# Kernel optimization log

Hardware: AMD Instinct MI355X
Metric: run time of the kernel (lower is better)

## Reference

```python
import jax, jax.numpy as jnp
import numpy as np


def _renorm(e):
    # torch Embedding max_norm=1: clip each looked-up vector to L2 norm <= 1
    n = jnp.linalg.norm(e, axis=-1, keepdims=True)
    return e * jnp.minimum(1.0, 1.0 / jnp.maximum(n, 1e-12))


def _lstm_last(x, lens, Wih, Whh, bih, bhh):
    # x: [N, T, D]; returns hidden state at step lens-1 per sequence
    N, T, D = x.shape
    tmask = jnp.arange(T)[None, :] < lens[:, None]  # [N, T]
    b = bih + bhh

    def step(carry, inp):
        h, c = carry
        xt, m = inp  # [N, D], [N]
        gates = xt @ Wih.T + h @ Whh.T + b
        i, f, g, o = jnp.split(gates, 4, axis=-1)
        c_new = jax.nn.sigmoid(f) * c + jax.nn.sigmoid(i) * jnp.tanh(g)
        h_new = jax.nn.sigmoid(o) * jnp.tanh(c_new)
        m = m[:, None]
        return (jnp.where(m, h_new, h), jnp.where(m, c_new, c)), None

    h0 = jnp.zeros((N, D), x.dtype)
    (hn, _), _ = jax.lax.scan(step, (h0, h0), (jnp.transpose(x, (1, 0, 2)), tmask.T))
    return hn


def _gat(feat, src, dst, idx_map, W, b, n_dst):
    # edge dot-product score + edge softmax over dst + weighted scatter-sum
    fd = feat[idx_map]                                   # [n_dst, D]
    score = jnp.sum(feat[src] * fd[dst], axis=-1)        # [E]
    m = jax.ops.segment_max(score, dst, num_segments=n_dst)
    w = jnp.exp(score - m[dst])
    z = jax.ops.segment_sum(w, dst, num_segments=n_dst)
    w = w / jnp.maximum(z[dst], 1e-12)
    agg = jax.ops.segment_sum(w[:, None] * feat[src], dst, num_segments=n_dst)
    rst = jax.nn.relu(agg @ W.T + b)
    return fd + rst  # residual=True


def setup_inputs() -> dict:
    key = jax.random.key(0)
    ks = jax.random.split(key, 24)
    D = 128
    N0, N1, N2 = 25600, 2560, 512
    E0, E1 = 25600, 5120
    T = 20
    NU, NI = 100000, 50000
    s = 0.05
    inp = {
        "user_emb": jax.random.normal(ks[0], (NU, D), jnp.float32),
        "item_emb": jax.random.normal(ks[1], (NI + 1, D), jnp.float32),
        "Wih": jax.random.normal(ks[2], (4 * D, D), jnp.float32) * s,
        "Whh": jax.random.normal(ks[3], (4 * D, D), jnp.float32) * s,
        "bih": jax.random.normal(ks[4], (4 * D,), jnp.float32) * s,
        "bhh": jax.random.normal(ks[5], (4 * D,), jnp.float32) * s,
        "W1": jax.random.normal(ks[6], (D, 2 * D), jnp.float32) * s,
        "gW0": jax.random.normal(ks[7], (D, D), jnp.float32) * s,
        "gb0": jax.random.normal(ks[8], (D,), jnp.float32) * s,
        "gW1": jax.random.normal(ks[9], (D, D), jnp.float32) * s,
        "gb1": jax.random.normal(ks[10], (D,), jnp.float32) * s,
        "W2": jax.random.normal(ks[11], (D, 2 * D), jnp.float32) * s,
        "uids": jax.random.randint(ks[12], (N0,), 0, NU, jnp.int32),
        "padded_seqs": jax.random.randint(ks[13], (N0, T), 0, NI + 1, jnp.int32),
        "lens": jax.random.randint(ks[14], (N0,), 1, T + 1, jnp.int32),
        "cur_sidx": jax.random.randint(ks[15], (N2,), 0, N0, jnp.int32),
        "src0": jax.random.randint(ks[16], (E0,), 0, N0, jnp.int32),
        "dst0": jax.random.randint(ks[17], (E0,), 0, N1, jnp.int32),
        "idx0": jax.random.randint(ks[18], (N1,), 0, N0, jnp.int32),
        "src1": jax.random.randint(ks[19], (E1,), 0, N1, jnp.int32),
        "dst1": jax.random.randint(ks[20], (E1,), 0, N2, jnp.int32),
        "idx1": jax.random.randint(ks[21], (N2,), 0, N1, jnp.int32),
    }
    return inp


def reference(user_emb, item_emb, Wih, Whh, bih, bhh, W1, gW0, gb0, gW1, gb1, W2,
              uids, padded_seqs, lens, cur_sidx, src0, dst0, idx0, src1, dst1, idx1):
    item_emb = item_emb.at[0].set(0.0)  # padding_idx=0
    emb_seqs = _renorm(item_emb[padded_seqs])             # [N0, T, D]
    hn = _lstm_last(emb_seqs, lens, Wih, Whh, bih, bhh)   # [N0, D] short-term
    long_term = _renorm(user_emb[uids])                   # [N0, D]
    cur = hn[cur_sidx]                                    # [B, D]
    feat = jax.nn.relu(jnp.concatenate([long_term, hn], axis=1) @ W1.T)
    feat = feat.at[cur_sidx].set(cur)
    feat = _gat(feat, src0, dst0, idx0, gW0, gb0, idx0.shape[0])
    feat = _gat(feat, src1, dst1, idx1, gW1, gb1, idx1.shape[0])
    sr = jnp.concatenate([cur, feat], axis=1) @ W2.T      # [B, D]
    logits = sr @ _renorm(item_emb[1:]).T                 # [B, num_items]
    return logits
```

## Files before the change

### kernel.cpp

```cpp
#include <hip/hip_runtime.h>
#include <hip/hip_bf16.h>

typedef __bf16 bf16x8 __attribute__((ext_vector_type(8)));
typedef float  f32x4  __attribute__((ext_vector_type(4)));

__device__ __forceinline__ float fastsig(float x){
  return __builtin_amdgcn_rcpf(1.f + __builtin_amdgcn_exp2f(-1.4426950408889634f * x));
}
__device__ __forceinline__ float fasttanh(float x){
  return 1.f - 2.f * __builtin_amdgcn_rcpf(__builtin_amdgcn_exp2f(2.8853900817779268f * x) + 1.f);
}

__device__ __forceinline__ unsigned encf(float f){
  unsigned u = __float_as_uint(f);
  return (u & 0x80000000u) ? ~u : (u | 0x80000000u);
}
__device__ __forceinline__ float decf(unsigned u){
  return __uint_as_float((u & 0x80000000u) ? (u ^ 0x80000000u) : ~u);
}

__device__ __forceinline__ int swzG(int row, int byteoff){ return ((row<<7) + byteoff) ^ ((row & 7) << 4); }

__global__ void init_kernel(unsigned* agg0, unsigned* agg1, unsigned* z0, unsigned* z1,
                            unsigned* m0, unsigned* m1, unsigned* hist){
  int g = blockIdx.x*256 + threadIdx.x;
  if      (g < 327680)                          agg0[g] = 0u;
  else if ((g -= 327680) < 65536)               agg1[g] = 0u;
  else if ((g -= 65536)  < 2560)                z0[g]   = 0u;
  else if ((g -= 2560)   < 512)                 z1[g]   = 0u;
  else if ((g -= 512)    < 2560)                m0[g]   = 0x00800000u;
  else if ((g -= 2560)   < 512)                 m1[g]   = 0x00800000u;
  else if ((g -= 512)    < 20)                  hist[g] = 0u;
}

__global__ void len_hist_kernel(const int* __restrict__ lens, int* __restrict__ hist, int n){
  __shared__ int lh[20];
  int t = threadIdx.x;
  if (t < 20) lh[t] = 0;
  __syncthreads();
  int i = blockIdx.x*256 + t;
  if (i < n) atomicAdd(&lh[lens[i]-1], 1);
  __syncthreads();
  if (t < 20 && lh[t] > 0) atomicAdd(&hist[t], lh[t]);
}
__global__ void len_prefix_kernel(const int* __restrict__ hist, int* __restrict__ offs){
  if (threadIdx.x == 0){
    int acc = 0;
    for (int i = 19; i >= 0; --i){ offs[i] = acc; acc += hist[i]; }
  }
}
__global__ void len_scatter_kernel(const int* __restrict__ lens, int* __restrict__ offs,
                                   int* __restrict__ perm, int n){
  __shared__ int cnt[20];
  __shared__ int base[20];
  int t = threadIdx.x;
  if (t < 20) cnt[t] = 0;
  __syncthreads();
  int i = blockIdx.x*256 + t;
  int bin = 0, rank = 0;
  if (i < n){
    bin = lens[i] - 1;
    rank = atomicAdd(&cnt[bin], 1);
  }
  __syncthreads();
  if (t < 20 && cnt[t] > 0) base[t] = atomicAdd(&offs[t], cnt[t]);
  __syncthreads();
  if (i < n) perm[base[bin] + rank] = i;
}

__global__ void prep_kernel(const float* __restrict__ Wih, const float* __restrict__ Whh,
                            const float* __restrict__ bih, const float* __restrict__ bhh,
                            const float* __restrict__ W1,
                            __bf16* __restrict__ Wcat, float* __restrict__ bias,
                            __bf16* __restrict__ W1b){
  int g = blockIdx.x*256 + threadIdx.x;
  if (g < 131072){
    int j = g >> 8, k = g & 255;
    float v = (k < 128) ? Wih[j*128 + k] : Whh[j*128 + (k-128)];
    Wcat[g] = (__bf16)v;
  } else if (g < 131584){
    int j = g - 131072;
    bias[j] = bih[j] + bhh[j];
  } else if (g < 164352){
    int q = g - 131584;
    W1b[q] = (__bf16)W1[q];
  }
}

__global__ void gather2_kernel(const float* __restrict__ item_emb, const float* __restrict__ user_emb,
                               const int* __restrict__ uids,
                               __bf16* __restrict__ itn, __bf16* __restrict__ A1){
  int r = blockIdx.x*4 + (threadIdx.x >> 6);
  if (r >= 75600) return;
  int lane = threadIdx.x & 63;
  const float* src;
  __bf16* dst;
  if (r < 50000){
    src = item_emb + (size_t)(r + 1)*128;
    dst = itn + (size_t)r*128;
  } else {
    int i = r - 50000;
    src = user_emb + (size_t)uids[i]*128;
    dst = A1 + (size_t)i*256;
  }
  float2 v = *(const float2*)(src + lane*2);
  float ss = v.x*v.x + v.y*v.y;
  #pragma unroll
  for (int m = 1; m < 64; m <<= 1) ss += __shfl_xor(ss, m);
  float scale = (ss > 1.f) ? (1.f/sqrtf(ss)) : 1.f;
  dst[lane*2]     = (__bf16)(v.x*scale);
  dst[lane*2 + 1] = (__bf16)(v.y*scale);
}

#define ROWB 528
__global__ __launch_bounds__(512, 1)
void lstm_kernel(const __bf16* __restrict__ itn, const int* __restrict__ seqs,
                 const __bf16* __restrict__ Wcat, const float* __restrict__ bias,
                 const int* __restrict__ lens, const int* __restrict__ perm,
                 __bf16* __restrict__ A1){
  __shared__ char Ab[64*ROWB];
  __shared__ float bsh[512];
  __shared__ int   llen[64];

  const int tid  = threadIdx.x;
  const int lane = tid & 63;
  const int wv   = tid >> 6;
  const int l15  = lane & 15;
  const int lq   = lane >> 4;
  const int n0   = blockIdx.x * 64;

  bsh[tid] = bias[tid];
  if (tid < 64) llen[tid] = lens[perm[n0 + tid]];

  const __bf16* wp[4];
  #pragma unroll
  for (int gi = 0; gi < 4; ++gi)
    wp[gi] = Wcat + (size_t)((gi*128 + wv*16 + l15)*256 + lq*8);

  const int xrow = tid >> 3;
  const int xsub = tid & 7;
  const int xwr  = xrow*ROWB + xsub*32;
  const int hwr  = xrow*ROWB + 256 + xsub*32;
  const int sidx = perm[n0 + xrow];

  __syncthreads();

  const int mxl = llen[0];
  int lens_p = 0;
  #pragma unroll
  for (int s = 0; s < 4; ++s)
    lens_p |= llen[s*16 + l15] << (8*s);

  float c[4][4];
  #pragma unroll
  for (int s = 0; s < 4; ++s)
    #pragma unroll
    for (int r = 0; r < 4; ++r) c[s][r] = 0.f;

  int rbs[4], hws[4];
  #pragma unroll
  for (int s = 0; s < 4; ++s){
    rbs[s] = (s*16 + l15)*ROWB + lq*16;
    hws[s] = (s*16 + l15)*ROWB + 256 + (wv*16 + lq*4)*2;
  }

  {
    const int4 z = {0,0,0,0};
    *(int4*)(Ab + hwr)      = z;
    *(int4*)(Ab + hwr + 16) = z;
    int idx0 = seqs[(size_t)sidx*20 + 0];
    int4 a = z, b = z;
    if (idx0 > 0){
      const __bf16* sp = itn + (size_t)(idx0-1)*128 + xsub*16;
      a = *(const int4*)(sp);
      b = *(const int4*)(sp + 8);
    }
    *(int4*)(Ab + xwr)      = a;
    *(int4*)(Ab + xwr + 16) = b;
  }
  int idx_next = seqs[(size_t)sidx*20 + 1];
  __syncthreads();

  for (int t = 0; t < mxl; ++t){
    int4 xq0 = {0,0,0,0}, xq1 = {0,0,0,0};
    const bool stage_next = (t + 1 < mxl);
    if (stage_next && idx_next > 0){
      const __bf16* sp = itn + (size_t)(idx_next-1)*128 + xsub*16;
      xq0 = *(const int4*)(sp);
      xq1 = *(const int4*)(sp + 8);
    }
    if (t + 2 < 20) idx_next = seqs[(size_t)sidx*20 + t + 2];

    f32x4 acc[4][4];
    #pragma unroll
    for (int gi = 0; gi < 4; ++gi){
      f32x4 bv = *(const f32x4*)(bsh + gi*128 + wv*16 + lq*4);
      #pragma unroll
      for (int s = 0; s < 4; ++s) acc[s][gi] = bv;
    }

    int4 s0[4], s1[4];
    #pragma unroll
    for (int gi = 0; gi < 4; ++gi) s0[gi] = *(const int4*)(wp[gi]);
    #pragma unroll
    for (int kk = 0; kk < 8; ++kk){
      if (kk < 7){
        if (kk & 1){
          #pragma unroll
          for (int gi = 0; gi < 4; ++gi) s0[gi] = *(const int4*)(wp[gi] + (kk+1)*32);
        } else {
          #pragma unroll
          for (int gi = 0; gi < 4; ++gi) s1[gi] = *(const int4*)(wp[gi] + (kk+1)*32);
        }
      }
      bf16x8 bfr[4];
      #pragma unroll
      for (int s = 0; s < 4; ++s)
        bfr[s] = __builtin_bit_cast(bf16x8, *(const int4*)(Ab + rbs[s] + kk*64));
      #pragma unroll
      for (int gi = 0; gi < 4; ++gi){
        bf16x8 wf = __builtin_bit_cast(bf16x8, (kk & 1) ? s1[gi] : s0[gi]);
        #pragma unroll
        for (int s = 0; s < 4; ++s)
          acc[s][gi] = __builtin_amdgcn_mfma_f32_16x16x32_bf16(wf, bfr[s], acc[s][gi], 0,0,0);
      }
    }

    float hv[4][4];
    #pragma unroll
    for (int s = 0; s < 4; ++s){
      const bool up = t < ((lens_p >> (8*s)) & 255);
      #pragma unroll
      for (int r = 0; r < 4; ++r){
        float cn = fastsig(acc[s][1][r])*c[s][r] + fastsig(acc[s][0][r])*fasttanh(acc[s][2][r]);
        hv[s][r] = fastsig(acc[s][3][r])*fasttanh(cn);
        if (up) c[s][r] = cn;
      }
    }

    __syncthreads();

    #pragma unroll
    for (int s = 0; s < 4; ++s){
      if (t < ((lens_p >> (8*s)) & 255)){
        union { __bf16 h[4]; int2 q; } u;
        #pragma unroll
        for (int r = 0; r < 4; ++r) u.h[r] = (__bf16)hv[s][r];
        *(int2*)(Ab + hws[s]) = u.q;
      }
    }
    if (stage_next){
      *(int4*)(Ab + xwr)      = xq0;
      *(int4*)(Ab + xwr + 16) = xq1;
    }
    __syncthreads();
  }

  {
    int4 a = *(const int4*)(Ab + hwr);
    int4 b = *(const int4*)(Ab + hwr + 16);
    __bf16* op = A1 + (size_t)sidx*256 + 128 + xsub*16;
    *(int4*)(op)     = a;
    *(int4*)(op + 8) = b;
  }
}

template<int RELU>
__global__ __launch_bounds__(256, 2)
void gemm_bt_kernel(const __bf16* __restrict__ A, const __bf16* __restrict__ B,
                    float* __restrict__ C, int M, int N, int K){
  __shared__ char As[16384];
  __shared__ char Bs[16384];
  const int tid  = threadIdx.x;
  const int lane = tid & 63;
  const int wv   = tid >> 6;
  const int wmw  = wv >> 1, wnw = wv & 1;
  const int l15  = lane & 15, lq = lane >> 4;
  const int n0 = blockIdx.x * 128;
  const int m0 = blockIdx.y * 128;

  f32x4 acc[4][4];
  #pragma unroll
  for (int a = 0; a < 4; ++a)
    #pragma unroll
    for (int b = 0; b < 4; ++b){ f32x4 z; z[0]=0.f;z[1]=0.f;z[2]=0.f;z[3]=0.f; acc[a][b]=z; }

  const int nkb = K >> 6;
  for (int kb = 0; kb < nkb; ++kb){
    __syncthreads();
    #pragma unroll
    for (int i = 0; i < 4; ++i){
      int c = tid + i*256;
      int row = c >> 3, kc = c & 7;
      int4 va = *(const int4*)(A + (size_t)(m0+row)*K + kb*64 + kc*8);
      *(int4*)(As + swzG(row, kc*16)) = va;
      int4 vb = {0,0,0,0};
      if (n0 + row < N) vb = *(const int4*)(B + (size_t)(n0+row)*K + kb*64 + kc*8);
      *(int4*)(Bs + swzG(row, kc*16)) = vb;
    }
    __syncthreads();
    #pragma unroll
    for (int ks = 0; ks < 2; ++ks){
      bf16x8 af[4], bfr[4];
      #pragma unroll
      for (int mi = 0; mi < 4; ++mi)
        af[mi] = __builtin_bit_cast(bf16x8, *(const int4*)(As + swzG(wmw*64 + mi*16 + l15, ks*64 + lq*16)));
      #pragma unroll
      for (int ni = 0; ni < 4; ++ni)
        bfr[ni] = __builtin_bit_cast(bf16x8, *(const int4*)(Bs + swzG(wnw*64 + ni*16 + l15, ks*64 + lq*16)));
      #pragma unroll
      for (int mi = 0; mi < 4; ++mi)
        #pragma unroll
        for (int ni = 0; ni < 4; ++ni)
          acc[mi][ni] = __builtin_amdgcn_mfma_f32_16x16x32_bf16(af[mi], bfr[ni], acc[mi][ni], 0,0,0);
    }
  }
  #pragma unroll
  for (int mi = 0; mi < 4; ++mi){
    #pragma unroll
    for (int ni = 0; ni < 4; ++ni){
      int col = n0 + wnw*64 + ni*16 + l15;
      if (col < N){
        #pragma unroll
        for (int r = 0; r < 4; ++r){
          int row = m0 + wmw*64 + mi*16 + lq*4 + r;
          float v = acc[mi][ni][r];
          if (RELU) v = fmaxf(v, 0.f);
          C[(size_t)row*N + col] = v;
        }
      }
    }
  }
}

__global__ void set_cur_kernel(const __bf16* __restrict__ A1, const int* __restrict__ cur_sidx,
                               float* __restrict__ feat){
  int g = blockIdx.x*256 + threadIdx.x;
  int i = g >> 7, d = g & 127;
  int row = cur_sidx[i];
  feat[(size_t)row*128 + d] = (float)A1[(size_t)row*256 + 128 + d];
}

__global__ void gat_score_kernel(const float* __restrict__ feat, const int* __restrict__ src,
                                 const int* __restrict__ dst, const int* __restrict__ idxm,
                                 float* __restrict__ score, unsigned* __restrict__ mbuf, int E){
  int e = blockIdx.x*4 + (threadIdx.x >> 6);
  if (e >= E) return;
  int lane = threadIdx.x & 63;
  int de = dst[e];
  const float2 a = *(const float2*)(feat + (size_t)src[e]*128 + lane*2);
  const float2 b = *(const float2*)(feat + (size_t)idxm[de]*128 + lane*2);
  float s = a.x*b.x + a.y*b.y;
  #pragma unroll
  for (int m = 1; m < 64; m <<= 1) s += __shfl_xor(s, m);
  if (lane == 0){
    score[e] = s;
    atomicMax(mbuf + de, encf(s));
  }
}

__global__ void gat_agg_kernel(const float* __restrict__ feat, const int* __restrict__ src,
                               const int* __restrict__ dst, const float* __restrict__ score,
                               const unsigned* __restrict__ mbuf,
                               float* __restrict__ agg, float* __restrict__ z, int E){
  int g = blockIdx.x*256 + threadIdx.x;
  int e = g >> 7, d = g & 127;
  if (e >= E) return;
  int de = dst[e];
  float w = __expf(score[e] - decf(mbuf[de]));
  if (d == 0) atomicAdd(z + de, w);
  atomicAdd(agg + (size_t)de*128 + d, w * feat[(size_t)src[e]*128 + d]);
}

__global__ void gat_out_kernel(const float* __restrict__ featPrev, const int* __restrict__ idxm,
                               const float* __restrict__ agg, const float* __restrict__ z,
                               const float* __restrict__ gW, const float* __restrict__ gb,
                               float* __restrict__ out, int V){
  __shared__ float arow[128];
  int v = blockIdx.x;
  int d = threadIdx.x;
  float zi = 1.f / fmaxf(z[v], 1e-12f);
  arow[d] = agg[(size_t)v*128 + d] * zi;
  __syncthreads();
  float s = gb[d];
  #pragma unroll 4
  for (int k = 0; k < 128; ++k) s += arow[k] * gW[d*128 + k];
  out[(size_t)v*128 + d] = featPrev[(size_t)idxm[v]*128 + d] + fmaxf(s, 0.f);
}

__global__ void sr_kernel(const __bf16* __restrict__ A1, const float* __restrict__ feat2,
                          const int* __restrict__ cur_sidx, const float* __restrict__ W2,
                          __bf16* __restrict__ srb){
  __shared__ float cat[256];
  int i = blockIdx.x;
  int j = threadIdx.x;
  int row = cur_sidx[i];
  cat[j]       = (float)A1[(size_t)row*256 + 128 + j];
  cat[128 + j] = feat2[(size_t)i*128 + j];
  __syncthreads();
  float s = 0.f;
  #pragma unroll 4
  for (int k = 0; k < 256; ++k) s += cat[k] * W2[j*256 + k];
  srb[(size_t)i*128 + j] = (__bf16)s;
}

extern "C" void kernel_launch(void* const* d_in, const int* in_sizes, int n_in,
                              void* d_out, int out_size, void* d_ws, size_t ws_size,
                              hipStream_t stream){
  const float* user_emb = (const float*)d_in[0];
  const float* item_emb = (const float*)d_in[1];
  const float* Wih = (const float*)d_in[2];
  const float* Whh = (const float*)d_in[3];
  const float* bih = (const float*)d_in[4];
  const float* bhh = (const float*)d_in[5];
  const float* W1  = (const float*)d_in[6];
  const float* gW0 = (const float*)d_in[7];
  const float* gb0 = (const float*)d_in[8];
  const float* gW1 = (const float*)d_in[9];
  const float* gb1 = (const float*)d_in[10];
  const float* W2  = (const float*)d_in[11];
  const int* uids = (const int*)d_in[12];
  const int* seqs = (const int*)d_in[13];
  const int* lens = (const int*)d_in[14];
  const int* cur_sidx = (const int*)d_in[15];
  const int* src0 = (const int*)d_in[16];
  const int* dst0 = (const int*)d_in[17];
  const int* idx0 = (const int*)d_in[18];
  const int* src1 = (const int*)d_in[19];
  const int* dst1 = (const int*)d_in[20];
  const int* idx1 = (const int*)d_in[21];
  float* out = (float*)d_out;

  char* ws = (char*)d_ws;
  size_t off = 0;
  auto alloc = [&](size_t bytes)->char* {
    char* p = ws + off;
    off += (bytes + 255) & ~((size_t)255);
    return p;
  };
  __bf16*   A1    = (__bf16*)  alloc(25600u*256*2);
  __bf16*   Wcat  = (__bf16*)  alloc(512u*256*2);
  float*    bias  = (float*)   alloc(512u*4);
  __bf16*   W1b   = (__bf16*)  alloc(128u*256*2);
  float*    feat  = (float*)   alloc(25600u*128*4);
  float*    sc0   = (float*)   alloc(25600u*4);
  unsigned* m0    = (unsigned*)alloc(2560u*4);
  float*    z0    = (float*)   alloc(2560u*4);
  float*    agg0  = (float*)   alloc(2560u*128*4);
  float*    feat1 = (float*)   alloc(2560u*128*4);
  float*    sc1   = (float*)   alloc(5120u*4);
  unsigned* m1    = (unsigned*)alloc(512u*4);
  float*    z1    = (float*)   alloc(512u*4);
  float*    agg1  = (float*)   alloc(512u*128*4);
  float*    feat2 = (float*)   alloc(512u*128*4);
  __bf16*   srb   = (__bf16*)  alloc(512u*128*2);
  __bf16*   itn   = (__bf16*)  alloc(50000u*128*2);
  int*      hist  = (int*)     alloc(20u*4);
  int*      offs  = (int*)     alloc(20u*4);
  int*      perm  = (int*)     alloc(25600u*4);

  prep_kernel<<<642, 256, 0, stream>>>(Wih, Whh, bih, bhh, W1, Wcat, bias, W1b);
  init_kernel<<<1561, 256, 0, stream>>>((unsigned*)agg0, (unsigned*)agg1, (unsigned*)z0,
                                        (unsigned*)z1, m0, m1, (unsigned*)hist);

  len_hist_kernel   <<<100, 256, 0, stream>>>(lens, hist, 25600);
  len_prefix_kernel <<<1,    64, 0, stream>>>(hist, offs);
  len_scatter_kernel<<<100, 256, 0, stream>>>(lens, offs, perm, 25600);

  gather2_kernel<<<18900, 256, 0, stream>>>(item_emb, user_emb, uids, itn, A1);

  lstm_kernel<<<400, 512, 0, stream>>>(itn, seqs, Wcat, bias, lens, perm, A1);

  gemm_bt_kernel<1><<<dim3(1, 200), 256, 0, stream>>>(A1, W1b, feat, 25600, 128, 256);
  set_cur_kernel<<<256, 256, 0, stream>>>(A1, cur_sidx, feat);

  gat_score_kernel<<<6400, 256, 0, stream>>>(feat, src0, dst0, idx0, sc0, m0, 25600);
  gat_agg_kernel  <<<12800,256, 0, stream>>>(feat, src0, dst0, sc0, m0, agg0, z0, 25600);
  gat_out_kernel  <<<2560, 128, 0, stream>>>(feat, idx0, agg0, z0, gW0, gb0, feat1, 2560);

  gat_score_kernel<<<1280, 256, 0, stream>>>(feat1, src1, dst1, idx1, sc1, m1, 5120);
  gat_agg_kernel  <<<2560, 256, 0, stream>>>(feat1, src1, dst1, sc1, m1, agg1, z1, 5120);
  gat_out_kernel  <<<512,  128, 0, stream>>>(feat1, idx1, agg1, z1, gW1, gb1, feat2, 512);

  sr_kernel<<<512, 128, 0, stream>>>(A1, feat2, cur_sidx, W2, srb);

  gemm_bt_kernel<0><<<dim3(391, 4), 256, 0, stream>>>(srb, itn, out, 512, 50000, 128);
}
```

Measured before the change: 265.2 us.

## Double-buffer LSTM shared state with swizzled layout to drop a barrier per step

The LSTM kernel now keeps two swizzled LDS buffers for the x/h operand and alternates between them each timestep. That removes the mid-step __syncthreads, and rows that are already finished copy their old h forward. The padded 528-byte row stride is replaced by an XOR swizzle against bank conflicts. Bias is now added after the MFMAs from global memory instead of LDS, and the first weight fragment is prefetched across steps. Max length comes from a wave shuffle rather than LDS. The cost is twice the LDS footprint, extra copy traffic for inactive rows, and repeated bias loads every step.

```diff
diff --git a/kernel.cpp b/kernel.cpp
--- a/kernel.cpp
+++ b/kernel.cpp
@@ -19,6 +19,7 @@
   return __uint_as_float((u & 0x80000000u) ? (u ^ 0x80000000u) : ~u);
 }
 
+__device__ __forceinline__ int swzA(int row, int byteoff){ return ((row<<9) + byteoff) ^ ((row & 7) << 4); }
 __device__ __forceinline__ int swzG(int row, int byteoff){ return ((row<<7) + byteoff) ^ ((row & 7) << 4); }
 
 __global__ void init_kernel(unsigned* agg0, unsigned* agg1, unsigned* z0, unsigned* z1,
@@ -112,15 +113,12 @@
   dst[lane*2 + 1] = (__bf16)(v.y*scale);
 }
 
-#define ROWB 528
 __global__ __launch_bounds__(512, 1)
 void lstm_kernel(const __bf16* __restrict__ itn, const int* __restrict__ seqs,
                  const __bf16* __restrict__ Wcat, const float* __restrict__ bias,
                  const int* __restrict__ lens, const int* __restrict__ perm,
                  __bf16* __restrict__ A1){
-  __shared__ char Ab[64*ROWB];
-  __shared__ float bsh[512];
-  __shared__ int   llen[64];
+  __shared__ char Ab[2][32768];
 
   const int tid  = threadIdx.x;
   const int lane = tid & 63;
@@ -129,45 +127,50 @@
   const int lq   = lane >> 4;
   const int n0   = blockIdx.x * 64;
 
-  bsh[tid] = bias[tid];
-  if (tid < 64) llen[tid] = lens[perm[n0 + tid]];
-
   const __bf16* wp[4];
   #pragma unroll
   for (int gi = 0; gi < 4; ++gi)
     wp[gi] = Wcat + (size_t)((gi*128 + wv*16 + l15)*256 + lq*8);
 
+  int lens_p = 0;
+  #pragma unroll
+  for (int s = 0; s < 4; ++s)
+    lens_p |= lens[perm[n0 + s*16 + l15]] << (8*s);
+  int mxl;
+  {
+    int m = max(max(lens_p & 255, (lens_p >> 8) & 255),
+                max((lens_p >> 16) & 255, (lens_p >> 24) & 255));
+    #pragma unroll
+    for (int o = 1; o < 16; o <<= 1) m = max(m, __shfl_xor(m, o));
+    mxl = m;
+  }
+
+  float c[4][4];
+  #pragma unroll
+  for (int s = 0; s < 4; ++s)
+    #pragma unroll
+    for (int r = 0; r < 4; ++r) c[s][r] = 0.f;
+
+  const int b64 = (l15 & 4) << 4;
+
+  int rbs[4], hws[4];
+  #pragma unroll
+  for (int s = 0; s < 4; ++s){
+    rbs[s] = swzA(s*16 + l15, lq*16) - b64;
+    hws[s] = swzA(s*16 + l15, 256 + (wv*16 + lq*4)*2);
+  }
   const int xrow = tid >> 3;
   const int xsub = tid & 7;
-  const int xwr  = xrow*ROWB + xsub*32;
-  const int hwr  = xrow*ROWB + 256 + xsub*32;
+  const int xwr0 = swzA(xrow, xsub*32);
+  const int xwr1 = swzA(xrow, xsub*32 + 16);
+  const int hwr0 = swzA(xrow, 256 + xsub*32);
+  const int hwr1 = swzA(xrow, 256 + xsub*32 + 16);
   const int sidx = perm[n0 + xrow];
-
-  __syncthreads();
-
-  const int mxl = llen[0];
-  int lens_p = 0;
-  #pragma unroll
-  for (int s = 0; s < 4; ++s)
-    lens_p |= llen[s*16 + l15] << (8*s);
-
-  float c[4][4];
-  #pragma unroll
-  for (int s = 0; s < 4; ++s)
-    #pragma unroll
-    for (int r = 0; r < 4; ++r) c[s][r] = 0.f;
-
-  int rbs[4], hws[4];
-  #pragma unroll
-  for (int s = 0; s < 4; ++s){
-    rbs[s] = (s*16 + l15)*ROWB + lq*16;
-    hws[s] = (s*16 + l15)*ROWB + 256 + (wv*16 + lq*4)*2;
-  }
 
   {
     const int4 z = {0,0,0,0};
-    *(int4*)(Ab + hwr)      = z;
-    *(int4*)(Ab + hwr + 16) = z;
+    *(int4*)(Ab[0] + hwr0) = z;
+    *(int4*)(Ab[0] + hwr1) = z;
     int idx0 = seqs[(size_t)sidx*20 + 0];
     int4 a = z, b = z;
     if (idx0 > 0){
@@ -175,13 +178,21 @@
       a = *(const int4*)(sp);
       b = *(const int4*)(sp + 8);
     }
-    *(int4*)(Ab + xwr)      = a;
-    *(int4*)(Ab + xwr + 16) = b;
+    *(int4*)(Ab[0] + xwr0) = a;
+    *(int4*)(Ab[0] + xwr1) = b;
   }
   int idx_next = seqs[(size_t)sidx*20 + 1];
+
+  int4 s0[4], s1[4];
+  #pragma unroll
+  for (int gi = 0; gi < 4; ++gi) s0[gi] = *(const int4*)(wp[gi]);
+
   __syncthreads();
 
   for (int t = 0; t < mxl; ++t){
+    const char* Bc = Ab[t & 1];
+    char*       Bn = Ab[(t & 1) ^ 1];
+
     int4 xq0 = {0,0,0,0}, xq1 = {0,0,0,0};
     const bool stage_next = (t + 1 < mxl);
     if (stage_next && idx_next > 0){
@@ -193,15 +204,10 @@
 
     f32x4 acc[4][4];
     #pragma unroll
-    for (int gi = 0; gi < 4; ++gi){
-      f32x4 bv = *(const f32x4*)(bsh + gi*128 + wv*16 + lq*4);
-      #pragma unroll
-      for (int s = 0; s < 4; ++s) acc[s][gi] = bv;
-    }
-
-    int4 s0[4], s1[4];
-    #pragma unroll
-    for (int gi = 0; gi < 4; ++gi) s0[gi] = *(const int4*)(wp[gi]);
+    for (int s = 0; s < 4; ++s)
+      #pragma unroll
+      for (int gi = 0; gi < 4; ++gi){ f32x4 z; z[0]=0.f;z[1]=0.f;z[2]=0.f;z[3]=0.f; acc[s][gi]=z; }
+
     #pragma unroll
     for (int kk = 0; kk < 8; ++kk){
       if (kk < 7){
@@ -213,10 +219,11 @@
           for (int gi = 0; gi < 4; ++gi) s1[gi] = *(const int4*)(wp[gi] + (kk+1)*32);
         }
       }
+      const int koff = (kk*64) ^ b64;
       bf16x8 bfr[4];
       #pragma unroll
       for (int s = 0; s < 4; ++s)
-        bfr[s] = __builtin_bit_cast(bf16x8, *(const int4*)(Ab + rbs[s] + kk*64));
+        bfr[s] = __builtin_bit_cast(bf16x8, *(const int4*)(Bc + rbs[s] + koff));
       #pragma unroll
       for (int gi = 0; gi < 4; ++gi){
         bf16x8 wf = __builtin_bit_cast(bf16x8, (kk & 1) ? s1[gi] : s0[gi]);
@@ -226,39 +233,49 @@
       }
     }
 
-    float hv[4][4];
-    #pragma unroll
-    for (int s = 0; s < 4; ++s){
-      const bool up = t < ((lens_p >> (8*s)) & 255);
-      #pragma unroll
-      for (int r = 0; r < 4; ++r){
-        float cn = fastsig(acc[s][1][r])*c[s][r] + fastsig(acc[s][0][r])*fasttanh(acc[s][2][r]);
-        hv[s][r] = fastsig(acc[s][3][r])*fasttanh(cn);
-        if (up) c[s][r] = cn;
-      }
-    }
-
-    __syncthreads();
+    if (stage_next){
+      #pragma unroll
+      for (int gi = 0; gi < 4; ++gi) s0[gi] = *(const int4*)(wp[gi]);
+    }
+
+    float bb[4][4];
+    #pragma unroll
+    for (int gi = 0; gi < 4; ++gi)
+      #pragma unroll
+      for (int r = 0; r < 4; ++r)
+        bb[gi][r] = bias[gi*128 + wv*16 + lq*4 + r];
 
     #pragma unroll
     for (int s = 0; s < 4; ++s){
       if (t < ((lens_p >> (8*s)) & 255)){
         union { __bf16 h[4]; int2 q; } u;
         #pragma unroll
-        for (int r = 0; r < 4; ++r) u.h[r] = (__bf16)hv[s][r];
-        *(int2*)(Ab + hws[s]) = u.q;
+        for (int r = 0; r < 4; ++r){
+          float ig = acc[s][0][r] + bb[0][r];
+          float fg = acc[s][1][r] + bb[1][r];
+          float gg = acc[s][2][r] + bb[2][r];
+          float og = acc[s][3][r] + bb[3][r];
+          float cn = fastsig(fg)*c[s][r] + fastsig(ig)*fasttanh(gg);
+          u.h[r] = (__bf16)(fastsig(og)*fasttanh(cn));
+          c[s][r] = cn;
+        }
+        *(int2*)(Bn + hws[s]) = u.q;
+      } else {
+        *(int2*)(Bn + hws[s]) = *(const int2*)(Bc + hws[s]);
       }
     }
+
     if (stage_next){
-      *(int4*)(Ab + xwr)      = xq0;
-      *(int4*)(Ab + xwr + 16) = xq1;
+      *(int4*)(Bn + xwr0) = xq0;
+      *(int4*)(Bn + xwr1) = xq1;
     }
     __syncthreads();
   }
 
   {
-    int4 a = *(const int4*)(Ab + hwr);
-    int4 b = *(const int4*)(Ab + hwr + 16);
+    const char* fb = Ab[mxl & 1];
+    int4 a = *(const int4*)(fb + hwr0);
+    int4 b = *(const int4*)(fb + hwr1);
     __bf16* op = A1 + (size_t)sidx*256 + 128 + xsub*16;
     *(int4*)(op)     = a;
     *(int4*)(op + 8) = b;
```

Measured after the change: 319.8 us. +20.6%, slower.

## Replace atomic GAT scatter with CSR-by-destination segment reduction fused into output

Applied to the files above, without the earlier changes.

Builds a destination-sorted edge order (histogram, prefix scan, scatter) for both GAT layers, then computes the segment max, softmax normaliser and weighted aggregation per destination node inside the output kernel. This removes the float atomicAdd scatter into agg/z, the atomicMax pass and the large zero-initialisation of agg buffers. In exchange it adds six small sort kernels and serial per-node edge loops whose length depends on degree skew.

```diff
diff --git a/kernel.cpp b/kernel.cpp
--- a/kernel.cpp
+++ b/kernel.cpp
@@ -11,26 +11,13 @@
   return 1.f - 2.f * __builtin_amdgcn_rcpf(__builtin_amdgcn_exp2f(2.8853900817779268f * x) + 1.f);
 }
 
-__device__ __forceinline__ unsigned encf(float f){
-  unsigned u = __float_as_uint(f);
-  return (u & 0x80000000u) ? ~u : (u | 0x80000000u);
-}
-__device__ __forceinline__ float decf(unsigned u){
-  return __uint_as_float((u & 0x80000000u) ? (u ^ 0x80000000u) : ~u);
-}
-
 __device__ __forceinline__ int swzG(int row, int byteoff){ return ((row<<7) + byteoff) ^ ((row & 7) << 4); }
 
-__global__ void init_kernel(unsigned* agg0, unsigned* agg1, unsigned* z0, unsigned* z1,
-                            unsigned* m0, unsigned* m1, unsigned* hist){
+__global__ void init_kernel(int* dh0, int* dh1, int* lhist){
   int g = blockIdx.x*256 + threadIdx.x;
-  if      (g < 327680)                          agg0[g] = 0u;
-  else if ((g -= 327680) < 65536)               agg1[g] = 0u;
-  else if ((g -= 65536)  < 2560)                z0[g]   = 0u;
-  else if ((g -= 2560)   < 512)                 z1[g]   = 0u;
-  else if ((g -= 512)    < 2560)                m0[g]   = 0x00800000u;
-  else if ((g -= 2560)   < 512)                 m1[g]   = 0x00800000u;
-  else if ((g -= 512)    < 20)                  hist[g] = 0u;
+  if      (g < 2560)            dh0[g]   = 0;
+  else if ((g -= 2560) < 512)   dh1[g]   = 0;
+  else if ((g -= 512)  < 20)    lhist[g] = 0;
 }
 
 __global__ void len_hist_kernel(const int* __restrict__ lens, int* __restrict__ hist, int n){
@@ -66,6 +53,55 @@
   if (t < 20 && cnt[t] > 0) base[t] = atomicAdd(&offs[t], cnt[t]);
   __syncthreads();
   if (i < n) perm[base[bin] + rank] = i;
+}
+
+__global__ void dst_hist_kernel(const int* __restrict__ dst, int* __restrict__ hist,
+                                int E, int nbins){
+  __shared__ int lh[2560];
+  int t = threadIdx.x;
+  for (int b = t; b < nbins; b += 256) lh[b] = 0;
+  __syncthreads();
+  int i = blockIdx.x*256 + t;
+  if (i < E) atomicAdd(&lh[dst[i]], 1);
+  __syncthreads();
+  for (int b = t; b < nbins; b += 256){ int v = lh[b]; if (v) atomicAdd(&hist[b], v); }
+}
+__global__ void dst_prefix_kernel(const int* __restrict__ hist, int* __restrict__ starts,
+                                  int* __restrict__ cur, int nbins){
+  __shared__ int wsum[4];
+  int t = threadIdx.x;
+  int per = nbins >> 8;
+  int base = t*per;
+  int loc = 0;
+  for (int i = 0; i < per; ++i) loc += hist[base+i];
+  int lane = t & 63, wid = t >> 6;
+  int scan = loc;
+  #pragma unroll
+  for (int o = 1; o < 64; o <<= 1){ int v = __shfl_up(scan, o); if (lane >= o) scan += v; }
+  if (lane == 63) wsum[wid] = scan;
+  __syncthreads();
+  int woff = 0;
+  for (int w = 0; w < wid; ++w) woff += wsum[w];
+  int run = woff + scan - loc;
+  for (int i = 0; i < per; ++i){
+    starts[base+i] = run; cur[base+i] = run; run += hist[base+i];
+  }
+  if (t == 255) starts[nbins] = run;
+}
+__global__ void dst_scatter_kernel(const int* __restrict__ dst, int* __restrict__ cur,
+                                   int* __restrict__ eord, int E, int nbins){
+  __shared__ int cnt[2560];
+  __shared__ int base[2560];
+  int t = threadIdx.x;
+  for (int b = t; b < nbins; b += 256) cnt[b] = 0;
+  __syncthreads();
+  int i = blockIdx.x*256 + t;
+  int bin = 0, rank = 0;
+  if (i < E){ bin = dst[i]; rank = atomicAdd(&cnt[bin], 1); }
+  __syncthreads();
+  for (int b = t; b < nbins; b += 256){ int v = cnt[b]; if (v) base[b] = atomicAdd(&cur[b], v); }
+  __syncthreads();
+  if (i < E) eord[base[bin] + rank] = i;
 }
 
 __global__ void prep_kernel(const float* __restrict__ Wih, const float* __restrict__ Whh,
@@ -343,7 +379,7 @@
 
 __global__ void gat_score_kernel(const float* __restrict__ feat, const int* __restrict__ src,
                                  const int* __restrict__ dst, const int* __restrict__ idxm,
-                                 float* __restrict__ score, unsigned* __restrict__ mbuf, int E){
+                                 float* __restrict__ score, int E){
   int e = blockIdx.x*4 + (threadIdx.x >> 6);
   if (e >= E) return;
   int lane = threadIdx.x & 63;
@@ -353,39 +389,33 @@
   float s = a.x*b.x + a.y*b.y;
   #pragma unroll
   for (int m = 1; m < 64; m <<= 1) s += __shfl_xor(s, m);
-  if (lane == 0){
-    score[e] = s;
-    atomicMax(mbuf + de, encf(s));
-  }
-}
-
-__global__ void gat_agg_kernel(const float* __restrict__ feat, const int* __restrict__ src,
-                               const int* __restrict__ dst, const float* __restrict__ score,
-                               const unsigned* __restrict__ mbuf,
-                               float* __restrict__ agg, float* __restrict__ z, int E){
-  int g = blockIdx.x*256 + threadIdx.x;
-  int e = g >> 7, d = g & 127;
-  if (e >= E) return;
-  int de = dst[e];
-  float w = __expf(score[e] - decf(mbuf[de]));
-  if (d == 0) atomicAdd(z + de, w);
-  atomicAdd(agg + (size_t)de*128 + d, w * feat[(size_t)src[e]*128 + d]);
-}
-
-__global__ void gat_out_kernel(const float* __restrict__ featPrev, const int* __restrict__ idxm,
-                               const float* __restrict__ agg, const float* __restrict__ z,
-                               const float* __restrict__ gW, const float* __restrict__ gb,
-                               float* __restrict__ out, int V){
+  if (lane == 0) score[e] = s;
+}
+
+__global__ void gat_fused_kernel(const float* __restrict__ feat, const int* __restrict__ src,
+                                 const int* __restrict__ idxm, const float* __restrict__ score,
+                                 const int* __restrict__ eord, const int* __restrict__ starts,
+                                 const float* __restrict__ gW, const float* __restrict__ gb,
+                                 float* __restrict__ out, int V){
   __shared__ float arow[128];
   int v = blockIdx.x;
   int d = threadIdx.x;
-  float zi = 1.f / fmaxf(z[v], 1e-12f);
-  arow[d] = agg[(size_t)v*128 + d] * zi;
+  int e0 = starts[v], e1 = starts[v+1];
+  float m = -3.4e38f;
+  for (int i = e0; i < e1; ++i) m = fmaxf(m, score[eord[i]]);
+  float z = 0.f, acc = 0.f;
+  for (int i = e0; i < e1; ++i){
+    int e = eord[i];
+    float w = __expf(score[e] - m);
+    z += w;
+    acc += w * feat[(size_t)src[e]*128 + d];
+  }
+  arow[d] = acc * (1.f / fmaxf(z, 1e-12f));
   __syncthreads();
   float s = gb[d];
   #pragma unroll 4
   for (int k = 0; k < 128; ++k) s += arow[k] * gW[d*128 + k];
-  out[(size_t)v*128 + d] = featPrev[(size_t)idxm[v]*128 + d] + fmaxf(s, 0.f);
+  out[(size_t)v*128 + d] = feat[(size_t)idxm[v]*128 + d] + fmaxf(s, 0.f);
 }
 
 __global__ void sr_kernel(const __bf16* __restrict__ A1, const float* __restrict__ feat2,
@@ -444,29 +474,37 @@
   __bf16*   W1b   = (__bf16*)  alloc(128u*256*2);
   float*    feat  = (float*)   alloc(25600u*128*4);
   float*    sc0   = (float*)   alloc(25600u*4);
-  unsigned* m0    = (unsigned*)alloc(2560u*4);
-  float*    z0    = (float*)   alloc(2560u*4);
-  float*    agg0  = (float*)   alloc(2560u*128*4);
   float*    feat1 = (float*)   alloc(2560u*128*4);
   float*    sc1   = (float*)   alloc(5120u*4);
-  unsigned* m1    = (unsigned*)alloc(512u*4);
-  float*    z1    = (float*)   alloc(512u*4);
-  float*    agg1  = (float*)   alloc(512u*128*4);
   float*    feat2 = (float*)   alloc(512u*128*4);
   __bf16*   srb   = (__bf16*)  alloc(512u*128*2);
   __bf16*   itn   = (__bf16*)  alloc(50000u*128*2);
   int*      hist  = (int*)     alloc(20u*4);
   int*      offs  = (int*)     alloc(20u*4);
   int*      perm  = (int*)     alloc(25600u*4);
+  int*      dh0   = (int*)     alloc(2560u*4);
+  int*      st0   = (int*)     alloc(2561u*4);
+  int*      cur0  = (int*)     alloc(2560u*4);
+  int*      eord0 = (int*)     alloc(25600u*4);
+  int*      dh1   = (int*)     alloc(512u*4);
+  int*      st1   = (int*)     alloc(513u*4);
+  int*      cur1  = (int*)     alloc(512u*4);
+  int*      eord1 = (int*)     alloc(5120u*4);
 
   prep_kernel<<<642, 256, 0, stream>>>(Wih, Whh, bih, bhh, W1, Wcat, bias, W1b);
-  init_kernel<<<1561, 256, 0, stream>>>((unsigned*)agg0, (unsigned*)agg1, (unsigned*)z0,
-                                        (unsigned*)z1, m0, m1, (unsigned*)hist);
+  init_kernel<<<13, 256, 0, stream>>>(dh0, dh1, hist);
 
   len_hist_kernel   <<<100, 256, 0, stream>>>(lens, hist, 25600);
   len_prefix_kernel <<<1,    64, 0, stream>>>(hist, offs);
   len_scatter_kernel<<<100, 256, 0, stream>>>(lens, offs, perm, 25600);
 
+  dst_hist_kernel   <<<100, 256, 0, stream>>>(dst0, dh0, 25600, 2560);
+  dst_prefix_kernel <<<1,   256, 0, stream>>>(dh0, st0, cur0, 2560);
+  dst_scatter_kernel<<<100, 256, 0, stream>>>(dst0, cur0, eord0, 25600, 2560);
+  dst_hist_kernel   <<<20,  256, 0, stream>>>(dst1, dh1, 5120, 512);
+  dst_prefix_kernel <<<1,   256, 0, stream>>>(dh1, st1, cur1, 512);
+  dst_scatter_kernel<<<20,  256, 0, stream>>>(dst1, cur1, eord1, 5120, 512);
+
   gather2_kernel<<<18900, 256, 0, stream>>>(item_emb, user_emb, uids, itn, A1);
 
   lstm_kernel<<<400, 512, 0, stream>>>(itn, seqs, Wcat, bias, lens, perm, A1);
@@ -474,13 +512,11 @@
   gemm_bt_kernel<1><<<dim3(1, 200), 256, 0, stream>>>(A1, W1b, feat, 25600, 128, 256);
   set_cur_kernel<<<256, 256, 0, stream>>>(A1, cur_sidx, feat);
 
-  gat_score_kernel<<<6400, 256, 0, stream>>>(feat, src0, dst0, idx0, sc0, m0, 25600);
-  gat_agg_kernel  <<<12800,256, 0, stream>>>(feat, src0, dst0, sc0, m0, agg0, z0, 25600);
-  gat_out_kernel  <<<2560, 128, 0, stream>>>(feat, idx0, agg0, z0, gW0, gb0, feat1, 2560);
-
-  gat_score_kernel<<<1280, 256, 0, stream>>>(feat1, src1, dst1, idx1, sc1, m1, 5120);
-  gat_agg_kernel  <<<2560, 256, 0, stream>>>(feat1, src1, dst1, sc1, m1, agg1, z1, 5120);
-  gat_out_kernel  <<<512,  128, 0, stream>>>(feat1, idx1, agg1, z1, gW1, gb1, feat2, 512);
+  gat_score_kernel<<<6400, 256, 0, stream>>>(feat, src0, dst0, idx0, sc0, 25600);
+  gat_fused_kernel<<<2560, 128, 0, stream>>>(feat, src0, idx0, sc0, eord0, st0, gW0, gb0, feat1, 2560);
+
+  gat_score_kernel<<<1280, 256, 0, stream>>>(feat1, src1, dst1, idx1, sc1, 5120);
+  gat_fused_kernel<<<512, 128, 0, stream>>>(feat1, src1, idx1, sc1, eord1, st1, gW1, gb1, feat2, 512);
 
   sr_kernel<<<512, 128, 0, stream>>>(A1, feat2, cur_sidx, W2, srb);
 
```

Result: slower. 271.6 us (+2.4%).
